# Kernel optimization log

Measured on AMD Instinct MI355X. Metric: run time of the kernel, lower is better.

## Reference

```python
import jax, jax.numpy as jnp
import numpy as np
import math

B, L, D = 4, 4096, 768          # batch, seq_len (== l_max), d_model
ORDER, EMB_DIM = 16, 3          # hyena_filter_order, hyena_emb_dim
W_MOD = 1.0                     # hyena_w_mod
FAST, SLOW, TARGET = 0.3, 1.5, 1e-2  # ExponentialModulation defaults


def setup_inputs() -> dict:
    key = jax.random.key(0)
    ks = jax.random.split(key, 16)
    n = lambda i, shape, s: jax.random.normal(ks[i], shape, dtype=jnp.float32) * s
    # PositionalEmbedding buffer/param z, deterministic Hyena init (seq_len = l_max = L)
    t = np.linspace(0.0, 1.0, L)[None, :, None]
    bands = (EMB_DIM - 1) // 2
    t_re = np.linspace(0, L - 1, L)[None, :, None]
    w = 2 * math.pi * t_re / L
    f = np.linspace(1e-4, bands - 1, bands)[None, None]
    zc = np.exp(-1j * f * w)
    z = np.concatenate([t, zc.real, zc.imag], axis=-1).astype(np.float32)  # (1, L, 3)
    return {
        "u": jax.random.normal(ks[0], (B, L, D), dtype=jnp.float32),
        "w_in": n(1, (3 * D, D), 0.02),
        "b_in": jnp.zeros((3 * D,), jnp.float32),
        "w_out": n(2, (D, D), 0.02),
        "b_out": jnp.zeros((D,), jnp.float32),
        "conv_w": n(3, (3 * D, 1, 3), 0.3),   # depthwise Conv1d weight (O, I/groups=1, K)
        "conv_b": jnp.zeros((3 * D,), jnp.float32),
        "z": jnp.asarray(z),
        "fw1": n(4, (ORDER, EMB_DIM), 0.3),
        "fb1": n(5, (ORDER,), 0.3),
        "fw2": n(6, (ORDER, ORDER), 0.3),
        "fb2": n(7, (ORDER,), 0.3),
        "fw3": n(8, (ORDER, ORDER), 0.3),
        "fb3": n(9, (ORDER,), 0.3),
        "fw4": n(10, (D, ORDER), 0.3),
        "freq": jnp.full((1, ORDER), 10.0, jnp.float32),  # shared Sin freq, init w*ones
        "filter_bias": jax.random.normal(ks[11], (D,), dtype=jnp.float32),
    }


def _hyena_filter(z, fw1, fb1, fw2, fb2, fw3, fb3, fw4, freq, Lq):
    # implicit MLP with SHARED Sin activation (same freq param at all 3 activations)
    sin = lambda h: jnp.sin(W_MOD * freq * h)
    h = sin(z @ fw1.T + fb1)
    h = sin(h @ fw2.T + fb2)
    h = sin(h @ fw3.T + fb3)
    h = h @ fw4.T                                     # (1, L, D)
    # ExponentialModulation
    max_d = math.log(TARGET) / FAST
    min_d = math.log(TARGET) / SLOW
    deltas = jnp.linspace(min_d, max_d, D)[None, None]  # (1, 1, D)
    t = jnp.linspace(0.0, 1.0, Lq)[None, :, None]       # (1, L, 1)
    h = h * jnp.exp(-t * jnp.abs(deltas))
    return h[0].T                                      # (D, L)


def _fftconv(v, k, bias):
    # causal FFT long conv: fft_size = 2L, torch norm='forward' conventions
    Lq = v.shape[-1]
    nfft = 2 * Lq
    k_f = jnp.fft.rfft(k, n=nfft) / nfft               # (D, nfft//2+1)
    v_f = jnp.fft.rfft(v, n=nfft)                      # (B, D, nfft//2+1)
    y = jnp.fft.irfft(v_f * k_f, n=nfft, norm="forward")[..., :Lq]
    return y + v * bias[None, :, None]


def reference(u, w_in, b_in, w_out, b_out, conv_w, conv_b, z,
              fw1, fb1, fw2, fb2, fw3, fb3, fw4, freq, filter_bias):
    Bq, Lq, Dq = u.shape
    x = u @ w_in.T + b_in                              # (B, L, 3D)
    x = x.transpose(0, 2, 1)                           # (B, 3D, L)
    # depthwise short conv, kernel 3, padding 2, sliced to [:L]
    xc = jax.lax.conv_general_dilated(
        x, conv_w, window_strides=(1,), padding=[(2, 2)],
        feature_group_count=3 * Dq,
        dimension_numbers=("NCH", "OIH", "NCH"))[..., :Lq]
    xc = xc + conv_b[None, :, None]
    x1, x2, v = jnp.split(xc, 3, axis=1)               # each (B, D, L)
    v = v * x1                                         # pre-gate
    k = _hyena_filter(z[:, :Lq], fw1, fb1, fw2, fb2, fw3, fb3, fw4, freq, Lq)
    y = _fftconv(v, k, filter_bias) * x2               # long conv + post-gate
    y = y.transpose(0, 2, 1) @ w_out.T + b_out         # (B, L, D)
    return y
```

## Files before the change

### kernel.cpp

```cpp
#include <hip/hip_runtime.h>

#define BB 4
#define LL 4096
#define DD 768
#define TD 2304
#define NFFT 8192
#define PI2 6.283185307179586f

__device__ __forceinline__ unsigned short f2b(float f) {
    unsigned u = __float_as_uint(f);
    unsigned r = (u + 0x7fffu + ((u >> 16) & 1u)) >> 16;
    return (unsigned short)r;
}
__device__ __forceinline__ float b2f(unsigned short h) {
    return __uint_as_float((unsigned)h << 16);
}
__device__ __forceinline__ unsigned cvt_pk_bf16(float lo, float hi) {
    unsigned r;
    asm("v_cvt_pk_bf16_f32 %0, %1, %2" : "=v"(r) : "v"(lo), "v"(hi));
    return r;
}

typedef __bf16 bf16x8 __attribute__((ext_vector_type(8)));
typedef float  f32x4  __attribute__((ext_vector_type(4)));

constexpr float TWC[16] = {
    1.f, 0.98078528f, 0.92387953f, 0.83146961f,
    0.70710678f, 0.55557023f, 0.38268343f, 0.19509032f,
    0.f, -0.19509032f, -0.38268343f, -0.55557023f,
    -0.70710678f, -0.83146961f, -0.92387953f, -0.98078528f};
constexpr float TWS[16] = {
    0.f, 0.19509032f, 0.38268343f, 0.55557023f,
    0.70710678f, 0.83146961f, 0.92387953f, 0.98078528f,
    1.f, 0.98078528f, 0.92387953f, 0.83146961f,
    0.70710678f, 0.55557023f, 0.38268343f, 0.19509032f};

template<int LOGN, bool INV>
__device__ __forceinline__ void reg_fft(float2* R) {
    constexpr int N = 1 << LOGN;
#pragma unroll
    for (int i = 0; i < N; ++i) {
        int j = 0;
#pragma unroll
        for (int b = 0; b < LOGN; ++b) if (i & (1 << b)) j |= (1 << (LOGN - 1 - b));
        if (j > i) { float2 tt = R[i]; R[i] = R[j]; R[j] = tt; }
    }
#pragma unroll
    for (int s = 1; s <= LOGN; ++s) {
        const int hm = 1 << (s - 1);
        const int tsh = 5 - s;
#pragma unroll
        for (int g = 0; g < N; g += (hm << 1)) {
#pragma unroll
            for (int j2 = 0; j2 < hm; ++j2) {
                const float wr = TWC[j2 << tsh];
                const float wi = INV ? TWS[j2 << tsh] : -TWS[j2 << tsh];
                float2 u = R[g + j2];
                float2 v = R[g + j2 + hm];
                float vr = v.x * wr - v.y * wi;
                float vi = v.x * wi + v.y * wr;
                R[g + j2]      = make_float2(u.x + vr, u.y + vi);
                R[g + j2 + hm] = make_float2(u.x - vr, u.y - vi);
            }
        }
    }
}

template<int NN>
__device__ __forceinline__ void ramp_mul(float2* R, float ang) {
    float s0, c0; __sincosf(ang, &s0, &c0);
    float wr = c0, wi = s0;
#pragma unroll
    for (int k = 1; k < NN; ++k) {
        float xr = R[k].x, xi = R[k].y;
        R[k] = make_float2(xr * wr - xi * wi, xr * wi + xi * wr);
        float nr = wr * c0 - wi * s0;
        float ni = wr * s0 + wi * c0;
        wr = nr; wi = ni;
    }
}

#define A1(t, k2) ((k2) * 288 + (t) + ((t) >> 3))
#define A2(k2, p, r) ((k2) * 272 + (r) * 17 + (p))
#define FFT_LDS 9216

__device__ __forceinline__ void eng_fwd(float2* buf, float2* R, int t) {
    reg_fft<5, false>(R);
    ramp_mul<32>(R, -PI2 * (float)t / 8192.0f);
    __syncthreads();
#pragma unroll
    for (int k2 = 0; k2 < 32; ++k2) buf[A1(t, k2)] = R[k2];
    __syncthreads();
    const int p = t & 15, c2 = (t >> 4) << 1;
#pragma unroll
    for (int q = 0; q < 16; ++q) {
        R[q]      = buf[A1(p + 16 * q, c2)];
        R[16 + q] = buf[A1(p + 16 * q, c2 + 1)];
    }
    reg_fft<4, false>(R);
    reg_fft<4, false>(R + 16);
    float a2 = -PI2 * (float)p / 256.0f;
    ramp_mul<16>(R, a2);
    ramp_mul<16>(R + 16, a2);
    __syncthreads();
#pragma unroll
    for (int r = 0; r < 16; ++r) {
        buf[A2(c2, p, r)]     = R[r];
        buf[A2(c2 + 1, p, r)] = R[16 + r];
    }
    __syncthreads();
    const int rr = p;
#pragma unroll
    for (int pp = 0; pp < 16; ++pp) {
        R[pp]      = buf[A2(c2, pp, rr)];
        R[16 + pp] = buf[A2(c2 + 1, pp, rr)];
    }
    reg_fft<4, false>(R);
    reg_fft<4, false>(R + 16);
}

__device__ __forceinline__ void eng_inv(float2* buf, float2* R, int t) {
    const int p = t & 15, c2 = (t >> 4) << 1, rr = p;
    reg_fft<4, true>(R);
    reg_fft<4, true>(R + 16);
    __syncthreads();
#pragma unroll
    for (int pp = 0; pp < 16; ++pp) {
        buf[A2(c2, pp, rr)]     = R[pp];
        buf[A2(c2 + 1, pp, rr)] = R[16 + pp];
    }
    __syncthreads();
#pragma unroll
    for (int r = 0; r < 16; ++r) {
        R[r]      = buf[A2(c2, p, r)];
        R[16 + r] = buf[A2(c2 + 1, p, r)];
    }
    float a2 = PI2 * (float)p / 256.0f;
    ramp_mul<16>(R, a2);
    ramp_mul<16>(R + 16, a2);
    reg_fft<4, true>(R);
    reg_fft<4, true>(R + 16);
    __syncthreads();
#pragma unroll
    for (int q = 0; q < 16; ++q) {
        buf[A1(p + 16 * q, c2)]     = R[q];
        buf[A1(p + 16 * q, c2 + 1)] = R[16 + q];
    }
    __syncthreads();
#pragma unroll
    for (int k2 = 0; k2 < 32; ++k2) R[k2] = buf[A1(t, k2)];
    ramp_mul<32>(R, PI2 * (float)t / 8192.0f);
    reg_fft<5, true>(R);
}

__global__ __launch_bounds__(256) void k_cast_pair(
        const float* __restrict__ srcA, unsigned long long nA4,
        const float* __restrict__ srcB, unsigned long long nB4,
        unsigned short* __restrict__ dstA, unsigned short* __restrict__ dstB) {
    unsigned long long i = (unsigned long long)blockIdx.x * 256 + threadIdx.x;
    const float* s; unsigned short* d;
    if (i < nA4)            { s = srcA + i * 4;         d = dstA + i * 4; }
    else if (i < nA4 + nB4) { unsigned long long j = i - nA4; s = srcB + j * 4; d = dstB + j * 4; }
    else return;
    float4 v = *(const float4*)s;
    unsigned long long p = (unsigned long long)f2b(v.x)
                         | ((unsigned long long)f2b(v.y) << 16)
                         | ((unsigned long long)f2b(v.z) << 32)
                         | ((unsigned long long)f2b(v.w) << 48);
    *(unsigned long long*)d = p;
}

#define GEMM_CORE                                                               \
    __shared__ unsigned char AsB[16384];                                        \
    __shared__ unsigned char BsB[16384];                                        \
    const int tid  = threadIdx.x;                                               \
    const int lane = tid & 63;                                                  \
    const int w    = tid >> 6;                                                  \
    const int wr   = w >> 1, wc = w & 1;                                        \
    const int nbx  = (int)gridDim.x;                                            \
    int bid = (int)blockIdx.y * nbx + (int)blockIdx.x;                          \
    { const int cpx = (nbx * (int)gridDim.y) >> 3;                              \
      bid = (bid & 7) * cpx + (bid >> 3); }                                     \
    const int m0 = (bid / nbx) * 128, n0 = (bid % nbx) * 128;                   \
    f32x4 acc[4][4] = {};                                                       \
    const int srow = lane >> 3;                    \
    const int sslot = (lane & 7) ^ srow;          \
    for (int k0 = 0; k0 < K; k0 += 64) {                                        \
        _Pragma("unroll")                                                       \
        for (int c = 0; c < 4; ++c) {                                           \
            int chunk = w * 4 + c;                                              \
            int row = chunk * 8 + srow;                                         \
            const char* ga = (const char*)A  + (((size_t)(m0 + row) * K + k0) * 2) + sslot * 16; \
            __builtin_amdgcn_global_load_lds(                                   \
                (const __attribute__((address_space(1))) void*)ga,              \
                (__attribute__((address_space(3))) void*)(AsB + chunk * 1024), 16, 0, 0); \
            const char* gb = (const char*)Bw + (((size_t)(n0 + row) * K + k0) * 2) + sslot * 16; \
            __builtin_amdgcn_global_load_lds(                                   \
                (const __attribute__((address_space(1))) void*)gb,              \
                (__attribute__((address_space(3))) void*)(BsB + chunk * 1024), 16, 0, 0); \
        }                                                                       \
        __syncthreads();                                                        \
        const int quad = lane >> 4;                                             \
        const int rsel = lane & 15;                                             \
        _Pragma("unroll")                                                       \
        for (int kk = 0; kk < 2; ++kk) {                                        \
            bf16x8 af[4], bfr[4];                                               \
            _Pragma("unroll")                                                   \
            for (int i = 0; i < 4; ++i) {                                       \
                int rowA = wr * 64 + i * 16 + rsel;                             \
                int slotA = (kk * 4 + quad) ^ (rsel & 7);                       \
                af[i]  = *(const bf16x8*)(AsB + rowA * 128 + slotA * 16);       \
                int rowB = wc * 64 + i * 16 + rsel;                             \
                bfr[i] = *(const bf16x8*)(BsB + rowB * 128 + slotA * 16);       \
            }                                                                   \
            _Pragma("unroll")                                                   \
            for (int i = 0; i < 4; ++i)                                         \
                _Pragma("unroll")                                               \
                for (int j = 0; j < 4; ++j)                                     \
                    acc[i][j] = __builtin_amdgcn_mfma_f32_16x16x32_bf16(af[i], bfr[j], acc[i][j], 0, 0, 0); \
        }                                                                       \
        __syncthreads();                                                        \
    }

__global__ __launch_bounds__(256) void k_gemm1_xt(
        const unsigned short* __restrict__ A, const unsigned short* __restrict__ Bw,
        const float* __restrict__ bias, unsigned short* __restrict__ xT,
        int K) {
    GEMM_CORE
    const int cq = lane >> 4;
    const int cn = lane & 15;
    const int b  = m0 >> 12;
    const int lb = (m0 & 4095) + wr * 64 + cq * 4;
#pragma unroll
    for (int j = 0; j < 4; ++j) {
        int col = n0 + wc * 64 + j * 16 + cn;
        float bv = bias[col];
        unsigned short* cp = xT + ((size_t)b * TD + col) * LL + lb;
#pragma unroll
        for (int i = 0; i < 4; ++i) {
            uint2 p;
            p.x = cvt_pk_bf16(acc[i][j][0] + bv, acc[i][j][1] + bv);
            p.y = cvt_pk_bf16(acc[i][j][2] + bv, acc[i][j][3] + bv);
            *(uint2*)(cp + i * 16) = p;
        }
    }
}

__global__ __launch_bounds__(256) void k_gemm_mfma(
        const unsigned short* __restrict__ A, const unsigned short* __restrict__ Bw,
        const float* __restrict__ bias, float* __restrict__ C,
        int N, int K) {
    GEMM_CORE
    const int cq = lane >> 4;
    const int cn = lane & 15;
#pragma unroll
    for (int j = 0; j < 4; ++j) {
        int col = n0 + wc * 64 + j * 16 + cn;
        float bv = bias[col];
#pragma unroll
        for (int i = 0; i < 4; ++i) {
            int rbase = m0 + wr * 64 + i * 16 + cq * 4;
#pragma unroll
            for (int r = 0; r < 4; ++r)
                C[(size_t)(rbase + r) * N + col] = acc[i][j][r] + bv;
        }
    }
}

__device__ __forceinline__ void ld_row18(const unsigned short* __restrict__ r,
                                         int l0, float* a) {
    unsigned ql = 0;
    if (l0 >= 2) ql = *(const unsigned*)(r + l0 - 2);
    a[0] = b2f((unsigned short)(ql & 0xffffu));
    a[1] = b2f((unsigned short)(ql >> 16));
    uint4 q0 = *(const uint4*)(r + l0);
    uint4 q1 = *(const uint4*)(r + l0 + 8);
    unsigned qq[8] = {q0.x, q0.y, q0.z, q0.w, q1.x, q1.y, q1.z, q1.w};
#pragma unroll
    for (int k2 = 0; k2 < 8; ++k2) {
        a[2 + 2 * k2] = b2f((unsigned short)(qq[k2] & 0xffffu));
        a[3 + 2 * k2] = b2f((unsigned short)(qq[k2] >> 16));
    }
}

#define SW(l) ((l) ^ (((l) >> 4) & 15))

__global__ __launch_bounds__(256) void k_convfft(
        const unsigned short* __restrict__ xT,
        const float* __restrict__ conv_w, const float* __restrict__ conv_b,
        const float2* __restrict__ kf,
        unsigned short* __restrict__ yg) {
    __shared__ float2 buf[FFT_LDS];
    const int bp = blockIdx.x;
    const int d = bp % DD;
    const int pair = bp / DD;
    const int b0 = pair * 2, b1 = b0 + 1;
    const int t = threadIdx.x;
    const int l0 = t << 4;
    const float w10 = conv_w[3*d],          w11 = conv_w[3*d+1],          w12 = conv_w[3*d+2];
    const float w20 = conv_w[3*(DD+d)],     w21 = conv_w[3*(DD+d)+1],     w22 = conv_w[3*(DD+d)+2];
    const float w30 = conv_w[3*(2*DD+d)],   w31 = conv_w[3*(2*DD+d)+1],   w32 = conv_w[3*(2*DD+d)+2];
    const float c1 = conv_b[d], c2 = conv_b[DD + d], c3 = conv_b[2*DD + d];
    float2*   vstage = buf;
    unsigned* xstage = (unsigned*)(buf + 4096);

    {
        float a[18], q1[16], vv[16];
        ld_row18(xT + ((size_t)b0 * TD + d) * LL, l0, a);
#pragma unroll
        for (int k = 0; k < 16; ++k) q1[k] = w10*a[k] + w11*a[k+1] + w12*a[k+2] + c1;
        ld_row18(xT + ((size_t)b0 * TD + 2*DD + d) * LL, l0, a);
#pragma unroll
        for (int k = 0; k < 16; ++k) vv[k] = (w30*a[k] + w31*a[k+1] + w32*a[k+2] + c3) * q1[k];
        ld_row18(xT + ((size_t)b1 * TD + d) * LL, l0, a);
#pragma unroll
        for (int k = 0; k < 16; ++k) q1[k] = w10*a[k] + w11*a[k+1] + w12*a[k+2] + c1;
        ld_row18(xT + ((size_t)b1 * TD + 2*DD + d) * LL, l0, a);
#pragma unroll
        for (int k = 0; k < 16; ++k)
            vstage[SW(l0 + k)] = make_float2(vv[k], (w30*a[k] + w31*a[k+1] + w32*a[k+2] + c3) * q1[k]);
        ld_row18(xT + ((size_t)b0 * TD + DD + d) * LL, l0, a);
#pragma unroll
        for (int k = 0; k < 16; ++k) q1[k] = w20*a[k] + w21*a[k+1] + w22*a[k+2] + c2;
        ld_row18(xT + ((size_t)b1 * TD + DD + d) * LL, l0, a);
#pragma unroll
        for (int k = 0; k < 16; ++k)
            xstage[SW(l0 + k)] = cvt_pk_bf16(q1[k], w20*a[k] + w21*a[k+1] + w22*a[k+2] + c2);
    }
    __syncthreads();
    float2 R[32];
    unsigned x2p[16];
#pragma unroll
    for (int j = 0; j < 16; ++j) {
        int idx = t + 256 * j;
        R[j] = vstage[SW(idx)];
        x2p[j] = xstage[SW(idx)];
        R[16 + j] = make_float2(0.f, 0.f);
    }
    eng_fwd(buf, R, t);
    const float2* kd = kf + (size_t)d * NFFT;
#pragma unroll
    for (int i = 0; i < 32; ++i) {
        float2 w = kd[i * 256 + t];
        float2 zv = R[i];
        R[i] = make_float2(zv.x * w.x - zv.y * w.y, zv.x * w.y + zv.y * w.x);
    }
    eng_inv(buf, R, t);
    unsigned short* o1 = yg + ((size_t)b0 * DD + d) * LL;
    unsigned short* o2 = o1 + (size_t)DD * LL;
#pragma unroll
    for (int j = 0; j < 16; ++j) {
        int idx = t + 256 * j;
        o1[idx] = f2b(R[j].x * b2f((unsigned short)(x2p[j] & 0xffffu)));
        o2[idx] = f2b(R[j].y * b2f((unsigned short)(x2p[j] >> 16)));
    }
}

__global__ __launch_bounds__(256) void k_filter_mlp(
        const float* __restrict__ z,
        const float* __restrict__ fw1, const float* __restrict__ fb1,
        const float* __restrict__ fw2, const float* __restrict__ fb2,
        const float* __restrict__ fw3, const float* __restrict__ fb3,
        const float* __restrict__ freq, float* __restrict__ h3g) {
    int l = blockIdx.x * 256 + threadIdx.x;
    float z0 = z[l*3+0], z1 = z[l*3+1], z2 = z[l*3+2];
    float h1[16], h2[16];
#pragma unroll
    for (int j = 0; j < 16; ++j) {
        float a = z0*fw1[j*3+0] + z1*fw1[j*3+1] + z2*fw1[j*3+2] + fb1[j];
        h1[j] = sinf(freq[j] * a);
    }
#pragma unroll
    for (int j = 0; j < 16; ++j) {
        float a = fb2[j];
#pragma unroll
        for (int i = 0; i < 16; ++i) a += h1[i] * fw2[j*16+i];
        h2[j] = sinf(freq[j] * a);
    }
#pragma unroll
    for (int j = 0; j < 16; ++j) {
        float a = fb3[j];
#pragma unroll
        for (int i = 0; i < 16; ++i) a += h2[i] * fw3[j*16+i];
        h3g[j * LL + l] = sinf(freq[j] * a);
    }
}

__global__ __launch_bounds__(256) void k_filter_fft(
        const float* __restrict__ h3g, const float* __restrict__ fw4,
        const float* __restrict__ fbias, float2* __restrict__ kf) {
    __shared__ float2 buf[FFT_LDS];
    const int d = blockIdx.x, t = threadIdx.x;
    float w4[16];
#pragma unroll
    for (int i = 0; i < 16; ++i) w4[i] = fw4[d * 16 + i];
    const float min_d = 3.070113457325394f;
    const float max_d = 15.35056728662697f;
    const float ad = min_d + (max_d - min_d) * ((float)d / 767.0f);
    float2 R[32];
#pragma unroll
    for (int j = 0; j < 16; ++j) {
        int l = t + 256 * j;
        float acc = 0.f;
#pragma unroll
        for (int i = 0; i < 16; ++i) acc += h3g[i * LL + l] * w4[i];
        acc *= __expf(-((float)l / 4095.0f) * ad);
        R[j] = make_float2(acc, 0.f);
        R[16 + j] = make_float2(0.f, 0.f);
    }
    eng_fwd(buf, R, t);
    const float fb = fbias[d];
    const float inv_n = 1.0f / (float)NFFT;
    float2* kd = kf + (size_t)d * NFFT;
#pragma unroll
    for (int i = 0; i < 32; ++i)
        kd[i * 256 + t] = make_float2((R[i].x + fb) * inv_n, R[i].y * inv_n);
}

__global__ __launch_bounds__(256) void k_transpose_cast(
        const unsigned short* __restrict__ yg, unsigned short* __restrict__ ygT) {
    __shared__ float t[64][65];
    const int b = blockIdx.z;
    const int d0 = blockIdx.y * 64;
    const int l0 = blockIdx.x * 64;
    for (int idx = threadIdx.x; idx < 4096; idx += 256) {
        int r = idx >> 6, c = idx & 63;
        t[r][c] = b2f(yg[((size_t)(b * DD + d0 + r)) * LL + l0 + c]);
    }
    __syncthreads();
    for (int idx = threadIdx.x; idx < 2048; idx += 256) {
        int r = idx >> 5, c = (idx & 31) * 2;
        unsigned int p = (unsigned int)f2b(t[c][r]) | ((unsigned int)f2b(t[c+1][r]) << 16);
        *(unsigned int*)&ygT[((size_t)(b * LL + l0 + r)) * DD + d0 + c] = p;
    }
}

extern "C" void kernel_launch(void* const* d_in, const int* in_sizes, int n_in,
                              void* d_out, int out_size, void* d_ws, size_t ws_size,
                              hipStream_t stream) {
    const float* u      = (const float*)d_in[0];
    const float* w_in   = (const float*)d_in[1];
    const float* b_in   = (const float*)d_in[2];
    const float* w_out  = (const float*)d_in[3];
    const float* b_out  = (const float*)d_in[4];
    const float* conv_w = (const float*)d_in[5];
    const float* conv_b = (const float*)d_in[6];
    const float* z      = (const float*)d_in[7];
    const float* fw1    = (const float*)d_in[8];
    const float* fb1    = (const float*)d_in[9];
    const float* fw2    = (const float*)d_in[10];
    const float* fb2    = (const float*)d_in[11];
    const float* fw3    = (const float*)d_in[12];
    const float* fb3    = (const float*)d_in[13];
    const float* fw4    = (const float*)d_in[14];
    const float* freq   = (const float*)d_in[15];
    const float* fbias  = (const float*)d_in[16];

    char* ws = (char*)d_ws;
    unsigned short* xT       = (unsigned short*)(ws);
    float2* kf               = (float2*)(ws + 75497472);
    float*  h3g              = (float*)(ws + 125829120);
    unsigned short* w_out_bf = (unsigned short*)(ws + 126091264);
    unsigned short* yg       = (unsigned short*)(ws + 127270912);
    unsigned short* ygT      = (unsigned short*)(ws + 152436736);
    unsigned short* u_bf     = (unsigned short*)(ws + 177602560);
    unsigned short* w_in_bf  = (unsigned short*)(ws + 202768384);

    k_cast_pair<<<(3145728 + 442368 + 255) / 256, 256, 0, stream>>>(
        u, 3145728ULL, w_in, 442368ULL, u_bf, w_in_bf);
    k_gemm1_xt<<<dim3(TD/128, (BB*LL)/128), 256, 0, stream>>>(u_bf, w_in_bf, b_in, xT, DD);
    k_filter_mlp<<<LL/256, 256, 0, stream>>>(z, fw1, fb1, fw2, fb2, fw3, fb3, freq, h3g);
    k_filter_fft<<<DD, 256, 0, stream>>>(h3g, fw4, fbias, kf);
    k_cast_pair<<<(147456 + 255) / 256, 256, 0, stream>>>(
        w_out, 147456ULL, (const float*)0, 0ULL, w_out_bf, (unsigned short*)0);
    k_convfft<<<(BB/2)*DD, 256, 0, stream>>>(xT, conv_w, conv_b, kf, yg);
    k_transpose_cast<<<dim3(LL/64, DD/64, BB), 256, 0, stream>>>(yg, ygT);
    k_gemm_mfma<<<dim3(DD/128, (BB*LL)/128), 256, 0, stream>>>(ygT, w_out_bf, b_out, (float*)d_out, DD, DD);
}
```

Measured before the change: 374.9 us.

## Fold w_out cast into input cast, regroup GEMM tiles, reorder convfft blocks

Merges the separate w_out bf16 cast launch into the first cast kernel, saving one kernel launch. Replaces the GEMM block swizzle with an XCD-aware mapping that groups 6 N-tiles per M-tile within each XCD, so L2 reuse of A and B tiles improves. Interleaves the two batch pairs per channel in k_convfft so the blocks sharing a filter spectrum run close together. Widens the transpose kernel's loads to 32-bit. The hardcoded group size of 6 assumes particular grid shapes (gemm1 has 18 column tiles, gemm2 has 6), so other shapes could map tiles incorrectly.

```diff
diff --git a/kernel.cpp b/kernel.cpp
--- a/kernel.cpp
+++ b/kernel.cpp
@@ -153,14 +153,17 @@
     reg_fft<5, true>(R);
 }
 
-__global__ __launch_bounds__(256) void k_cast_pair(
+__global__ __launch_bounds__(256) void k_cast3(
         const float* __restrict__ srcA, unsigned long long nA4,
         const float* __restrict__ srcB, unsigned long long nB4,
-        unsigned short* __restrict__ dstA, unsigned short* __restrict__ dstB) {
+        const float* __restrict__ srcC, unsigned long long nC4,
+        unsigned short* __restrict__ dstA, unsigned short* __restrict__ dstB,
+        unsigned short* __restrict__ dstC) {
     unsigned long long i = (unsigned long long)blockIdx.x * 256 + threadIdx.x;
     const float* s; unsigned short* d;
-    if (i < nA4)            { s = srcA + i * 4;         d = dstA + i * 4; }
-    else if (i < nA4 + nB4) { unsigned long long j = i - nA4; s = srcB + j * 4; d = dstB + j * 4; }
+    if (i < nA4)                  { s = srcA + i * 4;                       d = dstA + i * 4; }
+    else if (i < nA4 + nB4)       { unsigned long long j = i - nA4;         s = srcB + j * 4; d = dstB + j * 4; }
+    else if (i < nA4 + nB4 + nC4) { unsigned long long j = i - nA4 - nB4;   s = srcC + j * 4; d = dstC + j * 4; }
     else return;
     float4 v = *(const float4*)s;
     unsigned long long p = (unsigned long long)f2b(v.x)
@@ -178,10 +181,15 @@
     const int w    = tid >> 6;                                                  \
     const int wr   = w >> 1, wc = w & 1;                                        \
     const int nbx  = (int)gridDim.x;                                            \
-    int bid = (int)blockIdx.y * nbx + (int)blockIdx.x;                          \
-    { const int cpx = (nbx * (int)gridDim.y) >> 3;                              \
-      bid = (bid & 7) * cpx + (bid >> 3); }                                     \
-    const int m0 = (bid / nbx) * 128, n0 = (bid % nbx) * 128;                   \
+    const int bidl = (int)blockIdx.y * nbx + (int)blockIdx.x;                   \
+    const int cpx  = (nbx * (int)gridDim.y) >> 3;                               \
+    const int mpc  = cpx / nbx;                \
+    const int xcd  = bidl & 7;                                                  \
+    const int local = bidl >> 3;                                  \
+    const int sub  = local / (6 * mpc);                  \
+    const int rem  = local % (6 * mpc);                                         \
+    const int m0 = (xcd * mpc + rem / 6) * 128;                                 \
+    const int n0 = (sub * 6 + rem % 6) * 128;                                   \
     f32x4 acc[4][4] = {};                                                       \
     const int srow = lane >> 3;                    \
     const int sslot = (lane & 7) ^ srow;          \
@@ -292,8 +300,8 @@
         unsigned short* __restrict__ yg) {
     __shared__ float2 buf[FFT_LDS];
     const int bp = blockIdx.x;
-    const int d = bp % DD;
-    const int pair = bp / DD;
+    const int d = bp >> 1;
+    const int pair = bp & 1;
     const int b0 = pair * 2, b1 = b0 + 1;
     const int t = threadIdx.x;
     const int l0 = t << 4;
@@ -423,9 +431,11 @@
     const int b = blockIdx.z;
     const int d0 = blockIdx.y * 64;
     const int l0 = blockIdx.x * 64;
-    for (int idx = threadIdx.x; idx < 4096; idx += 256) {
-        int r = idx >> 6, c = idx & 63;
-        t[r][c] = b2f(yg[((size_t)(b * DD + d0 + r)) * LL + l0 + c]);
+    for (int idx = threadIdx.x; idx < 2048; idx += 256) {
+        int r = idx >> 5, c = (idx & 31) * 2;
+        unsigned q = *(const unsigned*)&yg[((size_t)(b * DD + d0 + r)) * LL + l0 + c];
+        t[r][c]     = b2f((unsigned short)(q & 0xffffu));
+        t[r][c + 1] = b2f((unsigned short)(q >> 16));
     }
     __syncthreads();
     for (int idx = threadIdx.x; idx < 2048; idx += 256) {
@@ -466,13 +476,11 @@
     unsigned short* u_bf     = (unsigned short*)(ws + 177602560);
     unsigned short* w_in_bf  = (unsigned short*)(ws + 202768384);
 
-    k_cast_pair<<<(3145728 + 442368 + 255) / 256, 256, 0, stream>>>(
-        u, 3145728ULL, w_in, 442368ULL, u_bf, w_in_bf);
+    k_cast3<<<(3145728 + 442368 + 147456 + 255) / 256, 256, 0, stream>>>(
+        u, 3145728ULL, w_in, 442368ULL, w_out, 147456ULL, u_bf, w_in_bf, w_out_bf);
     k_gemm1_xt<<<dim3(TD/128, (BB*LL)/128), 256, 0, stream>>>(u_bf, w_in_bf, b_in, xT, DD);
     k_filter_mlp<<<LL/256, 256, 0, stream>>>(z, fw1, fb1, fw2, fb2, fw3, fb3, freq, h3g);
     k_filter_fft<<<DD, 256, 0, stream>>>(h3g, fw4, fbias, kf);
-    k_cast_pair<<<(147456 + 255) / 256, 256, 0, stream>>>(
-        w_out, 147456ULL, (const float*)0, 0ULL, w_out_bf, (unsigned short*)0);
     k_convfft<<<(BB/2)*DD, 256, 0, stream>>>(xT, conv_w, conv_b, kf, yg);
     k_transpose_cast<<<dim3(LL/64, DD/64, BB), 256, 0, stream>>>(yg, ygT);
     k_gemm_mfma<<<dim3(DD/128, (BB*LL)/128), 256, 0, stream>>>(ygT, w_out_bf, b_out, (float*)d_out, DD, DD);
```

New measurement: 376.0 us. No clear change (+0.3%).
